# Kernel optimization log

Measured on AMD Instinct MI355X. Metric: run time of the kernel, lower is better.

Reference implementation:

```python
import jax, jax.numpy as jnp
import numpy as np


def _gcn_conv(h, src, dst, deg_inv_sqrt, W, b, num_nodes):
    # h: [N, Fin]; transform then normalized neighbor aggregation (incl. self-loops)
    h = h @ W  # [N, Fout]
    norm = deg_inv_sqrt[src] * deg_inv_sqrt[dst]  # [E+N]
    msgs = h[src] * norm[:, None]  # gather + scale
    out = jax.ops.segment_sum(msgs, dst, num_segments=num_nodes)
    return out + b


def setup_inputs() -> dict:
    key = jax.random.key(0)
    k1, k2, k3, k4 = jax.random.split(key, 4)
    N, E, F_IN, F_HID, F_OUT = 100000, 3200000, 1433, 16, 7
    x = jax.random.normal(k1, (N, F_IN), dtype=jnp.float32)
    edge_index = jax.random.randint(k2, (2, E), 0, N, dtype=jnp.int64)
    W1 = jax.random.normal(k3, (F_IN, F_HID), dtype=jnp.float32) * (1.0 / np.sqrt(F_IN))
    b1 = jnp.zeros((F_HID,), dtype=jnp.float32)
    W2 = jax.random.normal(k4, (F_HID, F_OUT), dtype=jnp.float32) * (1.0 / np.sqrt(F_HID))
    b2 = jnp.zeros((F_OUT,), dtype=jnp.float32)
    return {"x": x, "edge_index": edge_index, "W1": W1, "b1": b1, "W2": W2, "b2": b2}


def reference(x, edge_index, W1, b1, W2, b2):
    N = x.shape[0]
    # add self-loops (PyG GCNConv default)
    loops = jnp.arange(N, dtype=edge_index.dtype)
    src = jnp.concatenate([edge_index[0], loops])
    dst = jnp.concatenate([edge_index[1], loops])
    # symmetric normalization from in-degree over self-loop-augmented edges
    deg = jax.ops.segment_sum(jnp.ones_like(dst, dtype=x.dtype), dst, num_segments=N)
    deg_inv_sqrt = jnp.where(deg > 0, jax.lax.rsqrt(deg), 0.0)
    h = _gcn_conv(x, src, dst, deg_inv_sqrt, W1, b1, N)
    h = jax.nn.relu(h)
    # dropout is identity in eval mode (deterministic reference)
    h = _gcn_conv(h, src, dst, deg_inv_sqrt, W2, b2, N)
    return jax.nn.log_softmax(h, axis=1)
```

## Files before the change

kernel.cpp:

```cpp
#include <hip/hip_runtime.h>
#include <math.h>

#define F_IN 1433
#define F_HID 16
#define F_OUT 7
#define CAP 128
#define NSCAT 512
#define NKT 45
#define KTFULL 44

typedef __attribute__((ext_vector_type(8))) short bf16x8;
typedef __attribute__((ext_vector_type(4))) float f32x4;

__device__ __forceinline__ unsigned short f2bf(float f) {
  unsigned u = __float_as_uint(f);
  u += 0x7fffu + ((u >> 16) & 1u);
  return (unsigned short)(u >> 16);
}

__device__ __forceinline__ unsigned pk2(float a, float b) {
  return (unsigned)f2bf(a) | ((unsigned)f2bf(b) << 16);
}

__device__ __forceinline__ void upk_add(unsigned u, float& lo, float& hi) {
  lo += __uint_as_float(u << 16);
  hi += __uint_as_float(u & 0xffff0000u);
}

__global__ __launch_bounds__(256) void k_prep(const float* __restrict__ W1,
                                              int* __restrict__ cnt,
                                              uint4* __restrict__ W1f, int N,
                                              int nzb) {
  const int b = blockIdx.x, t = threadIdx.x;
  if (b < nzb) {
    const int i = b * 256 + t;
    if (i < N) cnt[i] = 0;
    return;
  }
  if (t >= 64) return;
  const int tile = b - nzb;
  const int kg = t >> 4, n = t & 15;
  unsigned u[4];
#pragma unroll
  for (int p = 0; p < 4; ++p) {
    const int k0 = tile * 32 + kg * 8 + 2 * p;
    const float a = (k0 < F_IN) ? W1[k0 * F_HID + n] : 0.0f;
    const float bb = (k0 + 1 < F_IN) ? W1[(k0 + 1) * F_HID + n] : 0.0f;
    u[p] = pk2(a, bb);
  }
  W1f[tile * 64 + t] = make_uint4(u[0], u[1], u[2], u[3]);
}

__global__ __launch_bounds__(256) void k_fused(
    const float* __restrict__ x, const uint4* __restrict__ W1f,
    const int* __restrict__ src, const int* __restrict__ dst,
    int* __restrict__ cnt, int* __restrict__ csr, float* __restrict__ h1f,
    int N, int E) {
  const int t = threadIdx.x;
  const int b = blockIdx.x;

  if (b < NSCAT) {
    const int ne4 = (E + 3) >> 2;
    for (int i4 = b * 256 + t; i4 < ne4; i4 += NSCAT * 256) {
      const int base = i4 * 4;
      if (base + 3 < E) {
        const int4 s = *(const int4*)(src + base);
        const int4 d = *(const int4*)(dst + base);
        int r;
        r = atomicAdd(&cnt[d.x], 1); csr[((size_t)d.x << 7) + r] = s.x;
        r = atomicAdd(&cnt[d.y], 1); csr[((size_t)d.y << 7) + r] = s.y;
        r = atomicAdd(&cnt[d.z], 1); csr[((size_t)d.z << 7) + r] = s.z;
        r = atomicAdd(&cnt[d.w], 1); csr[((size_t)d.w << 7) + r] = s.w;
      } else {
        for (int k = base; k < E; ++k) {
          const int d = dst[k];
          const int r = atomicAdd(&cnt[d], 1);
          csr[((size_t)d << 7) + r] = src[k];
        }
      }
    }
    return;
  }

  const int g = b - NSCAT;
  const int w = t >> 6;
  const int l = t & 63;
  const int mtile = g * 4 + w;
  const int row0 = mtile * 16;
  if (row0 >= N) return;
  const int m = l & 15;
  const int kg = l >> 4;
  int row = row0 + m;
  if (row >= N) row = N - 1;
  const float* __restrict__ xr = x + (size_t)row * F_IN;

  f32x4 acc = {0.f, 0.f, 0.f, 0.f};
  for (int kt = 0; kt < KTFULL; ++kt) {
    const int k0 = kt * 32 + kg * 8;
    const float4 xa = *(const float4*)(xr + k0);
    const float4 xb = *(const float4*)(xr + k0 + 4);
    union { unsigned u[4]; bf16x8 v; } av;
    av.u[0] = pk2(xa.x, xa.y);
    av.u[1] = pk2(xa.z, xa.w);
    av.u[2] = pk2(xb.x, xb.y);
    av.u[3] = pk2(xb.z, xb.w);
    union { uint4 q; bf16x8 v; } wv;
    wv.q = W1f[kt * 64 + l];
    acc = __builtin_amdgcn_mfma_f32_16x16x32_bf16(av.v, wv.v, acc, 0, 0, 0);
  }
  {
    const int k0 = KTFULL * 32 + kg * 8;
    float e[8];
#pragma unroll
    for (int j = 0; j < 8; ++j) {
      const int k = k0 + j;
      e[j] = (k < F_IN) ? xr[k] : 0.0f;
    }
    union { unsigned u[4]; bf16x8 v; } av;
    av.u[0] = pk2(e[0], e[1]);
    av.u[1] = pk2(e[2], e[3]);
    av.u[2] = pk2(e[4], e[5]);
    av.u[3] = pk2(e[6], e[7]);
    union { uint4 q; bf16x8 v; } wv;
    wv.q = W1f[KTFULL * 64 + l];
    acc = __builtin_amdgcn_mfma_f32_16x16x32_bf16(av.v, wv.v, acc, 0, 0, 0);
  }
#pragma unroll
  for (int r = 0; r < 4; ++r) {
    const int orow = row0 + kg * 4 + r;
    if (orow < N) h1f[(size_t)orow * F_HID + m] = acc[r];
  }
}

__global__ __launch_bounds__(256) void k_scale(const float4* __restrict__ h1f,
                                               const int* __restrict__ cnt,
                                               uint4* __restrict__ h1v, int N) {
  const int idx = blockIdx.x * 256 + threadIdx.x;
  if (idx >= 2 * N) return;
  const int node = idx >> 1;
  const float sc = rsqrtf((float)(cnt[node] + 1));
  const float4 a = h1f[idx * 2];
  const float4 b = h1f[idx * 2 + 1];
  uint4 o;
  o.x = pk2(a.x * sc, a.y * sc);
  o.y = pk2(a.z * sc, a.w * sc);
  o.z = pk2(b.x * sc, b.y * sc);
  o.w = pk2(b.z * sc, b.w * sc);
  h1v[idx] = o;
}

__device__ __forceinline__ void l1_finish(float a[8], int i, int d, int lane,
                                          int p, const uint4* __restrict__ h1v,
                                          const float* __restrict__ b1,
                                          const float* __restrict__ W2,
                                          uint4* __restrict__ h2v) {
#pragma unroll
  for (int m = 2; m <= 32; m <<= 1) {
#pragma unroll
    for (int j = 0; j < 8; ++j) a[j] += __shfl_xor(a[j], m);
  }
  const uint4 v = h1v[((size_t)i << 1) + p];
  upk_add(v.x, a[0], a[1]);
  upk_add(v.y, a[2], a[3]);
  upk_add(v.z, a[4], a[5]);
  upk_add(v.w, a[6], a[7]);
  const float sd = rsqrtf((float)(d + 1));
  const float4 bl = ((const float4*)b1)[p * 2];
  const float4 bh = ((const float4*)b1)[p * 2 + 1];
  float tt[8];
  tt[0] = fmaxf(fmaf(a[0], sd, bl.x), 0.f);
  tt[1] = fmaxf(fmaf(a[1], sd, bl.y), 0.f);
  tt[2] = fmaxf(fmaf(a[2], sd, bl.z), 0.f);
  tt[3] = fmaxf(fmaf(a[3], sd, bl.w), 0.f);
  tt[4] = fmaxf(fmaf(a[4], sd, bh.x), 0.f);
  tt[5] = fmaxf(fmaf(a[5], sd, bh.y), 0.f);
  tt[6] = fmaxf(fmaf(a[6], sd, bh.z), 0.f);
  tt[7] = fmaxf(fmaf(a[7], sd, bh.w), 0.f);
  const float* __restrict__ w = W2 + p * 8 * F_OUT;
  float o[F_OUT];
#pragma unroll
  for (int j = 0; j < F_OUT; ++j) {
    o[j] = tt[0] * w[0 * F_OUT + j] + tt[1] * w[1 * F_OUT + j] +
           tt[2] * w[2 * F_OUT + j] + tt[3] * w[3 * F_OUT + j] +
           tt[4] * w[4 * F_OUT + j] + tt[5] * w[5 * F_OUT + j] +
           tt[6] * w[6 * F_OUT + j] + tt[7] * w[7 * F_OUT + j];
  }
#pragma unroll
  for (int j = 0; j < F_OUT; ++j) o[j] += __shfl_xor(o[j], 1);
  if (lane == 0) {
    uint4 r;
    r.x = pk2(o[0] * sd, o[1] * sd);
    r.y = pk2(o[2] * sd, o[3] * sd);
    r.z = pk2(o[4] * sd, o[5] * sd);
    r.w = pk2(o[6] * sd, 0.0f);
    h2v[i] = r;
  }
}

__global__ __launch_bounds__(256) void k_agg1n(
    const int* __restrict__ cnt, const int* __restrict__ csr,
    const uint4* __restrict__ h1v, const float* __restrict__ b1,
    const float* __restrict__ W2, uint4* __restrict__ h2v, int N) {
  const int lane = threadIdx.x & 63;
  const int i0 = blockIdx.x * 8 + (threadIdx.x >> 6) * 2;
  if (i0 >= N) return;
  const int i1 = i0 + 1;
  const bool has1 = (i1 < N);
  const int nb = lane >> 1;
  const int p = lane & 1;

  const int d0 = cnt[i0];
  const int d1 = has1 ? cnt[i1] : 0;
  const int* __restrict__ row0 = csr + ((size_t)i0 << 7);
  const int* __restrict__ row1 = csr + ((size_t)i1 << 7);

  float A[8], B[8];
#pragma unroll
  for (int j = 0; j < 8; ++j) { A[j] = 0.f; B[j] = 0.f; }
  const int dm = max(d0, d1);
  for (int c0 = 0; c0 < dm; c0 += 32) {
    const int c = c0 + nb;
    if (c < d0) {
      const uint4 v = h1v[((size_t)row0[c] << 1) + p];
      upk_add(v.x, A[0], A[1]); upk_add(v.y, A[2], A[3]);
      upk_add(v.z, A[4], A[5]); upk_add(v.w, A[6], A[7]);
    }
    if (c < d1) {
      const uint4 v = h1v[((size_t)row1[c] << 1) + p];
      upk_add(v.x, B[0], B[1]); upk_add(v.y, B[2], B[3]);
      upk_add(v.z, B[4], B[5]); upk_add(v.w, B[6], B[7]);
    }
  }
  l1_finish(A, i0, d0, lane, p, h1v, b1, W2, h2v);
  if (has1) l1_finish(B, i1, d1, lane, p, h1v, b1, W2, h2v);
}

__device__ __forceinline__ void l2_finish(float a[8], int i, int d, int lane,
                                          const uint4* __restrict__ h2v,
                                          const float* __restrict__ b2,
                                          float* __restrict__ out) {
#pragma unroll
  for (int m = 1; m <= 32; m <<= 1) {
#pragma unroll
    for (int j = 0; j < 7; ++j) a[j] += __shfl_xor(a[j], m);
  }
  const uint4 v = h2v[i];
  upk_add(v.x, a[0], a[1]);
  upk_add(v.y, a[2], a[3]);
  upk_add(v.z, a[4], a[5]);
  float dummy = 0.f;
  upk_add(v.w, a[6], dummy);
  if (lane == 0) {
    const float sd = rsqrtf((float)(d + 1));
    float vv[7];
#pragma unroll
    for (int j = 0; j < 7; ++j) vv[j] = fmaf(a[j], sd, b2[j]);
    float m = fmaxf(fmaxf(fmaxf(vv[0], vv[1]), fmaxf(vv[2], vv[3])),
                    fmaxf(fmaxf(vv[4], vv[5]), vv[6]));
    float sum = 0.f;
#pragma unroll
    for (int j = 0; j < 7; ++j) sum += expf(vv[j] - m);
    const float l = m + logf(sum);
    float* __restrict__ op = out + (size_t)i * F_OUT;
#pragma unroll
    for (int j = 0; j < 7; ++j) op[j] = vv[j] - l;
  }
}

__global__ __launch_bounds__(256) void k_agg2n(const int* __restrict__ cnt,
                                               const int* __restrict__ csr,
                                               const uint4* __restrict__ h2v,
                                               const float* __restrict__ b2,
                                               float* __restrict__ out, int N) {
  const int lane = threadIdx.x & 63;
  const int i0 = blockIdx.x * 8 + (threadIdx.x >> 6) * 2;
  if (i0 >= N) return;
  const int i1 = i0 + 1;
  const bool has1 = (i1 < N);

  const int d0 = cnt[i0];
  const int d1 = has1 ? cnt[i1] : 0;
  const int* __restrict__ row0 = csr + ((size_t)i0 << 7);
  const int* __restrict__ row1 = csr + ((size_t)i1 << 7);

  float A[8], B[8];
#pragma unroll
  for (int j = 0; j < 8; ++j) { A[j] = 0.f; B[j] = 0.f; }
  const int dm = max(d0, d1);
  for (int c0 = 0; c0 < dm; c0 += 64) {
    const int c = c0 + lane;
    if (c < d0) {
      const uint4 v = h2v[row0[c]];
      upk_add(v.x, A[0], A[1]); upk_add(v.y, A[2], A[3]);
      upk_add(v.z, A[4], A[5]); upk_add(v.w, A[6], A[7]);
    }
    if (c < d1) {
      const uint4 v = h2v[row1[c]];
      upk_add(v.x, B[0], B[1]); upk_add(v.y, B[2], B[3]);
      upk_add(v.z, B[4], B[5]); upk_add(v.w, B[6], B[7]);
    }
  }
  l2_finish(A, i0, d0, lane, h2v, b2, out);
  if (has1) l2_finish(B, i1, d1, lane, h2v, b2, out);
}

extern "C" void kernel_launch(void* const* d_in, const int* in_sizes, int n_in,
                              void* d_out, int out_size, void* d_ws,
                              size_t ws_size, hipStream_t stream) {
  const float* x = (const float*)d_in[0];
  const int* ei = (const int*)d_in[1];
  const float* W1 = (const float*)d_in[2];
  const float* b1 = (const float*)d_in[3];
  const float* W2 = (const float*)d_in[4];
  const float* b2 = (const float*)d_in[5];

  const int N = in_sizes[0] / F_IN;
  const int E = in_sizes[1] / 2;
  const int* src = ei;
  const int* dst = ei + E;

  float* h1f = (float*)d_ws;
  unsigned short* h1b = (unsigned short*)(h1f + (size_t)16 * N);
  unsigned short* h2b = h1b + (size_t)16 * N;
  int* cnt = (int*)(h2b + (size_t)8 * N);
  int* csr = cnt + N;
  uint4* W1f = (uint4*)(csr + (size_t)N * CAP);
  float* out = (float*)d_out;

  const int B = 256;
  const int nzb = (N + B - 1) / B;
  const int ngb = ((N + 15) / 16 + 3) / 4;

  k_prep<<<nzb + NKT, B, 0, stream>>>(W1, cnt, W1f, N, nzb);
  k_fused<<<NSCAT + ngb, B, 0, stream>>>(x, W1f, src, dst, cnt, csr, h1f, N, E);
  k_scale<<<(2 * N + B - 1) / B, B, 0, stream>>>((const float4*)h1f, cnt,
                                                 (uint4*)h1b, N);
  k_agg1n<<<(N + 7) / 8, B, 0, stream>>>(cnt, csr, (const uint4*)h1b, b1, W2,
                                         (uint4*)h2b, N);
  k_agg2n<<<(N + 7) / 8, B, 0, stream>>>(cnt, csr, (const uint4*)h2b, b2, out,
                                         N);
}
```

Before: 410.3 us.

## Split fused scatter/GEMM kernel and compute two row tiles per wave

Splits the combined CSR-scatter and X@W1 kernel into two separate launches. The scatter now uses one thread per four edges instead of a fixed grid-stride pool, and the GEMM gives each wave 32 rows with two MFMA accumulators sharing each W1 fragment load. The goals are to cut W1 reloads, raise memory-level parallelism in the bandwidth-bound GEMM, and simplify scheduling. The cost is losing the overlap between the atomic scatter and the GEMM that the fused launch allowed, plus one extra kernel launch.

Measured after the change: 535.5 us. 30.5% more time.

```diff
diff --git a/kernel.cpp b/kernel.cpp
--- a/kernel.cpp
+++ b/kernel.cpp
@@ -5,7 +5,6 @@
 #define F_HID 16
 #define F_OUT 7
 #define CAP 128
-#define NSCAT 512
 #define NKT 45
 #define KTFULL 44
 
@@ -51,84 +50,102 @@
   W1f[tile * 64 + t] = make_uint4(u[0], u[1], u[2], u[3]);
 }
 
-__global__ __launch_bounds__(256) void k_fused(
-    const float* __restrict__ x, const uint4* __restrict__ W1f,
-    const int* __restrict__ src, const int* __restrict__ dst,
-    int* __restrict__ cnt, int* __restrict__ csr, float* __restrict__ h1f,
-    int N, int E) {
+__global__ __launch_bounds__(256) void k_scatter(const int* __restrict__ src,
+                                                 const int* __restrict__ dst,
+                                                 int* __restrict__ cnt,
+                                                 int* __restrict__ csr, int E) {
+  const int e4 = blockIdx.x * 256 + threadIdx.x;
+  const int base = e4 * 4;
+  if (base + 3 < E) {
+    const int4 s = *(const int4*)(src + base);
+    const int4 d = *(const int4*)(dst + base);
+    int r;
+    r = atomicAdd(&cnt[d.x], 1); csr[((size_t)d.x << 7) + r] = s.x;
+    r = atomicAdd(&cnt[d.y], 1); csr[((size_t)d.y << 7) + r] = s.y;
+    r = atomicAdd(&cnt[d.z], 1); csr[((size_t)d.z << 7) + r] = s.z;
+    r = atomicAdd(&cnt[d.w], 1); csr[((size_t)d.w << 7) + r] = s.w;
+  } else {
+    for (int k = base; k < E; ++k) {
+      const int d = dst[k];
+      const int r = atomicAdd(&cnt[d], 1);
+      csr[((size_t)d << 7) + r] = src[k];
+    }
+  }
+}
+
+__global__ __launch_bounds__(256) void k_gemm(const float* __restrict__ x,
+                                              const uint4* __restrict__ W1f,
+                                              float* __restrict__ h1f, int N) {
   const int t = threadIdx.x;
-  const int b = blockIdx.x;
-
-  if (b < NSCAT) {
-    const int ne4 = (E + 3) >> 2;
-    for (int i4 = b * 256 + t; i4 < ne4; i4 += NSCAT * 256) {
-      const int base = i4 * 4;
-      if (base + 3 < E) {
-        const int4 s = *(const int4*)(src + base);
-        const int4 d = *(const int4*)(dst + base);
-        int r;
-        r = atomicAdd(&cnt[d.x], 1); csr[((size_t)d.x << 7) + r] = s.x;
-        r = atomicAdd(&cnt[d.y], 1); csr[((size_t)d.y << 7) + r] = s.y;
-        r = atomicAdd(&cnt[d.z], 1); csr[((size_t)d.z << 7) + r] = s.z;
-        r = atomicAdd(&cnt[d.w], 1); csr[((size_t)d.w << 7) + r] = s.w;
-      } else {
-        for (int k = base; k < E; ++k) {
-          const int d = dst[k];
-          const int r = atomicAdd(&cnt[d], 1);
-          csr[((size_t)d << 7) + r] = src[k];
-        }
-      }
-    }
-    return;
-  }
-
-  const int g = b - NSCAT;
   const int w = t >> 6;
   const int l = t & 63;
-  const int mtile = g * 4 + w;
-  const int row0 = mtile * 16;
+  const int wid = blockIdx.x * 4 + w;
+  const int row0 = wid * 32;
   if (row0 >= N) return;
   const int m = l & 15;
   const int kg = l >> 4;
-  int row = row0 + m;
-  if (row >= N) row = N - 1;
-  const float* __restrict__ xr = x + (size_t)row * F_IN;
-
-  f32x4 acc = {0.f, 0.f, 0.f, 0.f};
+  int rowA = row0 + m;
+  int rowB = row0 + 16 + m;
+  if (rowA >= N) rowA = N - 1;
+  if (rowB >= N) rowB = N - 1;
+  const float* __restrict__ xa = x + (size_t)rowA * F_IN;
+  const float* __restrict__ xb = x + (size_t)rowB * F_IN;
+  const int koff = kg * 8;
+
+  f32x4 accA = {0.f, 0.f, 0.f, 0.f};
+  f32x4 accB = {0.f, 0.f, 0.f, 0.f};
   for (int kt = 0; kt < KTFULL; ++kt) {
-    const int k0 = kt * 32 + kg * 8;
-    const float4 xa = *(const float4*)(xr + k0);
-    const float4 xb = *(const float4*)(xr + k0 + 4);
-    union { unsigned u[4]; bf16x8 v; } av;
-    av.u[0] = pk2(xa.x, xa.y);
-    av.u[1] = pk2(xa.z, xa.w);
-    av.u[2] = pk2(xb.x, xb.y);
-    av.u[3] = pk2(xb.z, xb.w);
+    const int k0 = kt * 32 + koff;
+    const float4 a0 = *(const float4*)(xa + k0);
+    const float4 a1 = *(const float4*)(xa + k0 + 4);
+    const float4 b0 = *(const float4*)(xb + k0);
+    const float4 b1 = *(const float4*)(xb + k0 + 4);
+    const uint4 wq = W1f[kt * 64 + l];
     union { uint4 q; bf16x8 v; } wv;
-    wv.q = W1f[kt * 64 + l];
-    acc = __builtin_amdgcn_mfma_f32_16x16x32_bf16(av.v, wv.v, acc, 0, 0, 0);
+    wv.q = wq;
+    union { unsigned uu[4]; bf16x8 v; } av;
+    av.uu[0] = pk2(a0.x, a0.y);
+    av.uu[1] = pk2(a0.z, a0.w);
+    av.uu[2] = pk2(a1.x, a1.y);
+    av.uu[3] = pk2(a1.z, a1.w);
+    accA = __builtin_amdgcn_mfma_f32_16x16x32_bf16(av.v, wv.v, accA, 0, 0, 0);
+    union { unsigned uu[4]; bf16x8 v; } bv;
+    bv.uu[0] = pk2(b0.x, b0.y);
+    bv.uu[1] = pk2(b0.z, b0.w);
+    bv.uu[2] = pk2(b1.x, b1.y);
+    bv.uu[3] = pk2(b1.z, b1.w);
+    accB = __builtin_amdgcn_mfma_f32_16x16x32_bf16(bv.v, wv.v, accB, 0, 0, 0);
   }
   {
-    const int k0 = KTFULL * 32 + kg * 8;
-    float e[8];
+    const int k0 = KTFULL * 32 + koff;
+    float ea[8], eb[8];
 #pragma unroll
     for (int j = 0; j < 8; ++j) {
       const int k = k0 + j;
-      e[j] = (k < F_IN) ? xr[k] : 0.0f;
-    }
-    union { unsigned u[4]; bf16x8 v; } av;
-    av.u[0] = pk2(e[0], e[1]);
-    av.u[1] = pk2(e[2], e[3]);
-    av.u[2] = pk2(e[4], e[5]);
-    av.u[3] = pk2(e[6], e[7]);
+      ea[j] = (k < F_IN) ? xa[k] : 0.0f;
+      eb[j] = (k < F_IN) ? xb[k] : 0.0f;
+    }
     union { uint4 q; bf16x8 v; } wv;
     wv.q = W1f[KTFULL * 64 + l];
-    acc = __builtin_amdgcn_mfma_f32_16x16x32_bf16(av.v, wv.v, acc, 0, 0, 0);
+    union { unsigned uu[4]; bf16x8 v; } av;
+    av.uu[0] = pk2(ea[0], ea[1]);
+    av.uu[1] = pk2(ea[2], ea[3]);
+    av.uu[2] = pk2(ea[4], ea[5]);
+    av.uu[3] = pk2(ea[6], ea[7]);
+    accA = __builtin_amdgcn_mfma_f32_16x16x32_bf16(av.v, wv.v, accA, 0, 0, 0);
+    union { unsigned uu[4]; bf16x8 v; } bv;
+    bv.uu[0] = pk2(eb[0], eb[1]);
+    bv.uu[1] = pk2(eb[2], eb[3]);
+    bv.uu[2] = pk2(eb[4], eb[5]);
+    bv.uu[3] = pk2(eb[6], eb[7]);
+    accB = __builtin_amdgcn_mfma_f32_16x16x32_bf16(bv.v, wv.v, accB, 0, 0, 0);
   }
 #pragma unroll
   for (int r = 0; r < 4; ++r) {
-    const int orow = row0 + kg * 4 + r;
-    if (orow < N) h1f[(size_t)orow * F_HID + m] = acc[r];
+    const int oa = row0 + kg * 4 + r;
+    if (oa < N) h1f[(size_t)oa * F_HID + m] = accA[r];
+    const int ob = row0 + 16 + kg * 4 + r;
+    if (ob < N) h1f[(size_t)ob * F_HID + m] = accB[r];
   }
 }
 
@@ -329,10 +346,12 @@
 
   const int B = 256;
   const int nzb = (N + B - 1) / B;
-  const int ngb = ((N + 15) / 16 + 3) / 4;
+  const int ne4 = (E + 3) / 4;
+  const int ngb = ((N + 31) / 32 + 3) / 4;
 
   k_prep<<<nzb + NKT, B, 0, stream>>>(W1, cnt, W1f, N, nzb);
-  k_fused<<<NSCAT + ngb, B, 0, stream>>>(x, W1f, src, dst, cnt, csr, h1f, N, E);
+  k_scatter<<<(ne4 + B - 1) / B, B, 0, stream>>>(src, dst, cnt, csr, E);
+  k_gemm<<<ngb, B, 0, stream>>>(x, W1f, h1f, N);
   k_scale<<<(2 * N + B - 1) / B, B, 0, stream>>>((const float4*)h1f, cnt,
                                                  (uint4*)h1b, N);
   k_agg1n<<<(N + 7) / 8, B, 0, stream>>>(cnt, csr, (const uint4*)h1b, b1, W2,
```

## Stage x tiles into LDS with double-buffered global_load_lds in fused GEMM

Applied to the files above, without the earlier changes.

The first-layer GEMM now stages 64-row by 32-column tiles of x into LDS using gfx950's direct global-to-LDS 16-byte loads. It double-buffers them with an XOR swizzle to avoid bank conflicts, and each block now covers 64 rows. The goal is better coalescing of the streaming x read and overlap of the next tile's fetch with the current MFMA. In exchange it adds a block-wide barrier every k-step and 16KB of static LDS, which also applies to the scatter blocks in the same kernel.

Result: no change. 414.4 us (+1.0%).

```diff
diff --git a/kernel.cpp b/kernel.cpp
--- a/kernel.cpp
+++ b/kernel.cpp
@@ -9,8 +9,15 @@
 #define NKT 45
 #define KTFULL 44
 
+#define AS1 __attribute__((address_space(1)))
+#define AS3 __attribute__((address_space(3)))
+
 typedef __attribute__((ext_vector_type(8))) short bf16x8;
 typedef __attribute__((ext_vector_type(4))) float f32x4;
+
+__device__ __forceinline__ void gload_lds16(const float* gp, float* lp) {
+  __builtin_amdgcn_global_load_lds((const AS1 void*)gp, (AS3 void*)lp, 16, 0, 0);
+}
 
 __device__ __forceinline__ unsigned short f2bf(float f) {
   unsigned u = __float_as_uint(f);
@@ -56,6 +63,7 @@
     const int* __restrict__ src, const int* __restrict__ dst,
     int* __restrict__ cnt, int* __restrict__ csr, float* __restrict__ h1f,
     int N, int E) {
+  __shared__ float xs[2 * 2048];
   const int t = threadIdx.x;
   const int b = blockIdx.x;
 
@@ -83,32 +91,54 @@
   }
 
   const int g = b - NSCAT;
+  const int row0g = g * 64;
+  if (row0g >= N) return;
   const int w = t >> 6;
   const int l = t & 63;
-  const int mtile = g * 4 + w;
-  const int row0 = mtile * 16;
-  if (row0 >= N) return;
   const int m = l & 15;
   const int kg = l >> 4;
-  int row = row0 + m;
-  if (row >= N) row = N - 1;
-  const float* __restrict__ xr = x + (size_t)row * F_IN;
+
+  const int s_swz = (l & 7) ^ (l >> 3);
+
+#define STAGE(BUF, KT)                                                       \
+  do {                                                                       \
+    _Pragma("unroll") for (int r_ = 0; r_ < 2; ++r_) {                       \
+      const int rloc_ = w * 8 + (l >> 3) + r_ * 32;                          \
+      const int grow_ = row0g + rloc_;                                       \
+      float* lp_ = xs + (BUF) * 2048 + r_ * 1024 + w * 256;                  \
+      if (grow_ < N)                                                         \
+        gload_lds16(x + (size_t)grow_ * F_IN + (KT) * 32 + s_swz * 4, lp_);  \
+    }                                                                        \
+  } while (0)
 
   f32x4 acc = {0.f, 0.f, 0.f, 0.f};
+  const int rloc = w * 16 + m;
+  const int c0 = (2 * kg) ^ (m & 7);
+  const int c1 = (2 * kg + 1) ^ (m & 7);
+
+  STAGE(0, 0);
+  __syncthreads();
   for (int kt = 0; kt < KTFULL; ++kt) {
-    const int k0 = kt * 32 + kg * 8;
-    const float4 xa = *(const float4*)(xr + k0);
-    const float4 xb = *(const float4*)(xr + k0 + 4);
-    union { unsigned u[4]; bf16x8 v; } av;
-    av.u[0] = pk2(xa.x, xa.y);
-    av.u[1] = pk2(xa.z, xa.w);
-    av.u[2] = pk2(xb.x, xb.y);
-    av.u[3] = pk2(xb.z, xb.w);
+    const int cur = kt & 1;
+    if (kt + 1 < KTFULL) STAGE(cur ^ 1, kt + 1);
+    const float* xrow = xs + cur * 2048 + rloc * 32;
+    const float4 fa = *(const float4*)(xrow + c0 * 4);
+    const float4 fb = *(const float4*)(xrow + c1 * 4);
+    union { unsigned uu[4]; bf16x8 v; } av;
+    av.uu[0] = pk2(fa.x, fa.y);
+    av.uu[1] = pk2(fa.z, fa.w);
+    av.uu[2] = pk2(fb.x, fb.y);
+    av.uu[3] = pk2(fb.z, fb.w);
     union { uint4 q; bf16x8 v; } wv;
     wv.q = W1f[kt * 64 + l];
     acc = __builtin_amdgcn_mfma_f32_16x16x32_bf16(av.v, wv.v, acc, 0, 0, 0);
-  }
+    __syncthreads();
+  }
+#undef STAGE
   {
+    int rowA = row0g + w * 16 + m;
+    if (rowA >= N) rowA = N - 1;
+    const float* __restrict__ xr = x + (size_t)rowA * F_IN;
     const int k0 = KTFULL * 32 + kg * 8;
     float e[8];
 #pragma unroll
@@ -116,18 +146,18 @@
       const int k = k0 + j;
       e[j] = (k < F_IN) ? xr[k] : 0.0f;
     }
-    union { unsigned u[4]; bf16x8 v; } av;
-    av.u[0] = pk2(e[0], e[1]);
-    av.u[1] = pk2(e[2], e[3]);
-    av.u[2] = pk2(e[4], e[5]);
-    av.u[3] = pk2(e[6], e[7]);
+    union { unsigned uu[4]; bf16x8 v; } av;
+    av.uu[0] = pk2(e[0], e[1]);
+    av.uu[1] = pk2(e[2], e[3]);
+    av.uu[2] = pk2(e[4], e[5]);
+    av.uu[3] = pk2(e[6], e[7]);
     union { uint4 q; bf16x8 v; } wv;
     wv.q = W1f[KTFULL * 64 + l];
     acc = __builtin_amdgcn_mfma_f32_16x16x32_bf16(av.v, wv.v, acc, 0, 0, 0);
   }
 #pragma unroll
   for (int r = 0; r < 4; ++r) {
-    const int orow = row0 + kg * 4 + r;
+    const int orow = row0g + w * 16 + kg * 4 + r;
     if (orow < N) h1f[(size_t)orow * F_HID + m] = acc[r];
   }
 }
@@ -329,7 +359,7 @@
 
   const int B = 256;
   const int nzb = (N + B - 1) / B;
-  const int ngb = ((N + 15) / 16 + 3) / 4;
+  const int ngb = (N + 63) / 64;
 
   k_prep<<<nzb + NKT, B, 0, stream>>>(W1, cnt, W1f, N, nzb);
   k_fused<<<NSCAT + ngb, B, 0, stream>>>(x, W1f, src, dst, cnt, csr, h1f, N, E);
```
